# Optimization experiments

Measured on AMD Instinct MI355X. Metric: run time of the kernel, lower is better.

## Reference

```python
import jax, jax.numpy as jnp
import numpy as np

D = 8        # q_ndim (= dof_ndim)
HID = 200    # hidden_size
N = 16384    # batch of states
EPS = 0.1    # qdot regularizer coefficient in L()


def _lagrangian(z, Ws, bs):
    # z: (2D,) = [q, qdot]; angular_dims=() so CosSin is an identity pass-through
    v = z[D:]
    h = z
    for W, b in zip(Ws[:-1], bs[:-1]):
        h = jax.nn.softplus(h @ W + b)   # FCsoftplus blocks
    L = (h @ Ws[-1] + bs[-1])[0]          # final Linear -> scalar (Reshape(-1))
    return L + EPS * jnp.dot(v, v)


def setup_inputs():
    key = jax.random.key(0)
    ks = jax.random.split(key, 5)
    z = jax.random.normal(ks[0], (N, 2 * D), dtype=jnp.float32)
    t = jnp.zeros((), dtype=jnp.float32)

    def lin(k, fi, fo, scale):
        return (jax.random.normal(k, (fi, fo), dtype=jnp.float32)
                * jnp.float32(scale / np.sqrt(fi)))

    W0 = lin(ks[1], 2 * D, HID, 1.0)
    W1 = lin(ks[2], HID, HID, 1.0)
    W2 = lin(ks[3], HID, HID, 1.0)
    W3 = lin(ks[4], HID, 1, 0.01)  # small head keeps mass matrix M well conditioned
    b0 = jnp.zeros((HID,), jnp.float32)  # zero_bias init per FCsoftplus/Linear
    b1 = jnp.zeros((HID,), jnp.float32)
    b2 = jnp.zeros((HID,), jnp.float32)
    b3 = jnp.zeros((1,), jnp.float32)
    return dict(t=t, z=z, W0=W0, b0=b0, W1=W1, b1=b1, W2=W2, b2=b2, W3=W3, b3=b3)


def reference(t, z, W0, b0, W1, b1, W2, b2, W3, b3):
    # Euler-Lagrange dynamics (LagrangianDynamics):
    #   M a = dL/dq - (d2L/dq dv) v,  M = d2L/dv2;  dz/dt = [v, a]
    Ws = (W0, W1, W2, W3)
    bs = (b0, b1, b2, b3)
    Lfn = lambda zz: _lagrangian(zz, Ws, bs)

    def dyn_single(zi):
        g = jax.grad(Lfn)(zi)              # (2D,)  = [dL/dq, dL/dv]
        H = jax.jacfwd(jax.grad(Lfn))(zi)  # (2D,2D) Hessian of L wrt z
        v = zi[D:]
        M = H[D:, D:]                      # d(dL/dv)/dv  -> mass matrix
        C = H[D:, :D]                      # d(dL/dv)/dq
        F = g[:D] - C @ v
        a = jnp.linalg.solve(M, F)
        return jnp.concatenate([v, a])     # (2D,)

    return jax.vmap(dyn_single)(z)         # (N, 2D)
```

## Files before the change

kernel.cpp:

```cpp
#include <hip/hip_runtime.h>
#include <math.h>

#define DD 8
#define ZD 16
#define HID 200
#define EPSL 0.1f
#define BS 16
#define NTHREADS 512
#define NKC 7
#define NMT 13
#define XSTR 216
#define CSTR 212
#define HSTR 20
#define NTAN 8

#define KSC 1024.0f
#define SSC 64.0f
#define INV_K (1.0f/1024.0f)
#define INV_KS (1.0f/65536.0f)

typedef _Float16 half8 __attribute__((ext_vector_type(8)));
typedef _Float16 half4v __attribute__((ext_vector_type(4)));
typedef float float4v __attribute__((ext_vector_type(4)));

#define S4 (NKC*NMT*64*8)
#define OFF_W1T 0
#define OFF_W2T (S4)
#define OFF_W1  (2*S4)
#define OFF_W2  (3*S4)
#define OFF_W0T (4*S4)
#define OFF_W0  (4*S4 + NMT*64*8)
#define WS_HALFS (4*S4 + NMT*64*8 + NKC*64*8)

__global__ void prep(const float* __restrict__ W0, const float* __restrict__ W1,
                     const float* __restrict__ W2, _Float16* __restrict__ ws)
{
    int idx = blockIdx.x * 256 + threadIdx.x;
    if (idx >= WS_HALFS) return;
    float v = 0.f;
    if (idx < 4*S4) {
        int arr = idx / S4, e = idx % S4;
        int kc = e / (NMT*64*8); int r = e % (NMT*64*8);
        int mt = r / (64*8); r %= 64*8;
        int lane = r / 8, j = r % 8;
        int m = mt*16 + (lane & 15);
        int k = kc*32 + (lane >> 4)*8 + j;
        if (m < HID && k < HID) {
            if      (arr == 0) v = W1[k*HID + m];
            else if (arr == 1) v = W2[k*HID + m];
            else if (arr == 2) v = W1[m*HID + k];
            else               v = W2[m*HID + k];
        }
    } else if (idx < OFF_W0) {
        int e = idx - OFF_W0T;
        int mt = e / (64*8); int r = e % (64*8);
        int lane = r / 8, j = r % 8;
        int m = mt*16 + (lane & 15);
        int k = (lane >> 4)*8 + j;
        if (m < HID && k < ZD) v = W0[k*HID + m];
    } else {
        int e = idx - OFF_W0;
        int kc = e / (64*8); int r = e % (64*8);
        int lane = r / 8, j = r % 8;
        int m = (lane & 15);
        int k = kc*32 + (lane >> 4)*8 + j;
        if (k < HID) v = W0[m*HID + k];
    }
    ws[idx] = (_Float16)v;
}

__device__ __forceinline__ float4v ldc4(const _Float16* p) {
    half4v h = *(const half4v*)p;
    float4v f; f.x = (float)h.x; f.y = (float)h.y; f.z = (float)h.z; f.w = (float)h.w;
    return f;
}
__device__ __forceinline__ void sth4(_Float16* p, float a, float b, float c, float d) {
    half4v h; h.x = (_Float16)a; h.y = (_Float16)b; h.z = (_Float16)c; h.w = (_Float16)d;
    *(half4v*)p = h;
}
__device__ __forceinline__ void sig_sp(float x, float& sp, float& sg) {
    float e = __expf(-fabsf(x));
    float r = 1.0f / (1.0f + e);
    sg = (x >= 0.f) ? r : (1.0f - r);
    sp = fmaxf(x, 0.f) + __logf(1.f + e);
}

template<int NTILES>
__device__ __forceinline__ void run_mv(const half8* __restrict__ Asw,
                                       const _Float16* Xsrc,
                                       int mt0, int mtc, int lane,
                                       float4v acc[2][NTILES])
{
    const int lm = lane & 15, q = lane >> 4;
#pragma unroll
    for (int m = 0; m < 2; ++m)
#pragma unroll
        for (int n = 0; n < NTILES; ++n)
            acc[m][n] = (float4v){0.f, 0.f, 0.f, 0.f};
    for (int kc = 0; kc < NKC; ++kc) {
        half8 a[2];
#pragma unroll
        for (int m = 0; m < 2; ++m)
            if (m < mtc) a[m] = Asw[(kc*NMT + mt0 + m)*64 + lane];
        half8 x[NTILES];
#pragma unroll
        for (int n = 0; n < NTILES; ++n)
            x[n] = *(const half8*)(Xsrc + (n*16 + lm)*XSTR + kc*32 + q*8);
#pragma unroll
        for (int m = 0; m < 2; ++m)
            if (m < mtc)
#pragma unroll
                for (int n = 0; n < NTILES; ++n)
                    acc[m][n] = __builtin_amdgcn_mfma_f32_16x16x32_f16(a[m], x[n], acc[m][n], 0, 0, 0);
    }
}

__global__ void __launch_bounds__(NTHREADS, 1)
lnn_main(const float* __restrict__ z,
         const float* __restrict__ W0, const float* __restrict__ b0,
         const float* __restrict__ b1, const float* __restrict__ b2,
         const float* __restrict__ W3,
         const _Float16* __restrict__ ws,
         float* __restrict__ out)
{
    __shared__ _Float16 Xt[128*XSTR];
    __shared__ _Float16 Xb[128*XSTR];
    __shared__ _Float16 Cf[5][16*CSTR];
    __shared__ _Float16 Xz[16*40];
    __shared__ float gsh[16*HSTR];
    __shared__ float Hr[128*HSTR];

    const int tid  = threadIdx.x;
    const int wave = tid >> 6;
    const int lane = tid & 63;
    const int lm   = lane & 15;
    const int q    = lane >> 4;
    const int s0   = blockIdx.x * BS;

    const int mt0 = (wave < 5) ? wave*2 : (10 + (wave - 5));
    const int mtc = (wave < 5) ? 2 : 1;

    const half8* W1Tsw = (const half8*)(ws + OFF_W1T);
    const half8* W2Tsw = (const half8*)(ws + OFF_W2T);
    const half8* W1sw  = (const half8*)(ws + OFF_W1);
    const half8* W2sw  = (const half8*)(ws + OFF_W2);
    const half8* W0Tsw = (const half8*)(ws + OFF_W0T);
    const half8* W0sw  = (const half8*)(ws + OFF_W0);

    {
        if (tid < 256) {
            int s = tid >> 4, k = tid & 15;
            Xz[s*40 + k]      = (_Float16)z[(s0 + s)*ZD + k];
            Xz[s*40 + 16 + k] = (_Float16)0.f;
        }
        for (int idx = tid; idx < 128*16; idx += NTHREADS) {
            int r = idx >> 4, c = 200 + (idx & 15);
            Xt[r*XSTR + c] = (_Float16)0.f;
            Xb[r*XSTR + c] = (_Float16)0.f;
        }
    }
    __syncthreads();

    float4v acc1[2][1];

    {
#pragma unroll
        for (int m = 0; m < 2; ++m) acc1[m][0] = (float4v){0.f,0.f,0.f,0.f};
        half8 xz = *(const half8*)(Xz + lm*40 + q*8);
#pragma unroll
        for (int m = 0; m < 2; ++m)
            if (m < mtc) {
                half8 a = W0Tsw[(mt0 + m)*64 + lane];
                acc1[m][0] = __builtin_amdgcn_mfma_f32_16x16x32_f16(a, xz, acc1[m][0], 0, 0, 0);
            }
#pragma unroll
        for (int m = 0; m < 2; ++m)
            if (m < mtc) {
                int mt = mt0 + m, ub = mt*16 + q*4;
                bool pad = (mt == 12 && q >= 2);
                float4v bb = *(const float4v*)(b0 + ub);
                float h[4], p[4];
#pragma unroll
                for (int r = 0; r < 4; ++r) {
                    float a = acc1[m][0][r] + bb[r];
                    float sp, sg; sig_sp(a, sp, sg);
                    h[r] = pad ? 0.f : sp;
                    p[r] = pad ? 0.f : sg;
                }
                sth4(&Xt[lm*XSTR + ub], h[0], h[1], h[2], h[3]);
                sth4(&Cf[0][lm*CSTR + ub], p[0], p[1], p[2], p[3]);
            }
    }
    __syncthreads();

    run_mv<1>(W1Tsw, Xt, mt0, mtc, lane, acc1);
    __syncthreads();
#pragma unroll
    for (int m = 0; m < 2; ++m)
        if (m < mtc) {
            int mt = mt0 + m, ub = mt*16 + q*4;
            bool pad = (mt == 12 && q >= 2);
            float4v bb = *(const float4v*)(b1 + ub);
            float h[4], p[4];
#pragma unroll
            for (int r = 0; r < 4; ++r) {
                float a = acc1[m][0][r] + bb[r];
                float sp, sg; sig_sp(a, sp, sg);
                h[r] = pad ? 0.f : sp;
                p[r] = pad ? 0.f : sg;
            }
            sth4(&Xt[lm*XSTR + ub], h[0], h[1], h[2], h[3]);
            sth4(&Cf[1][lm*CSTR + ub], p[0], p[1], p[2], p[3]);
        }
    __syncthreads();

    run_mv<1>(W2Tsw, Xt, mt0, mtc, lane, acc1);
    __syncthreads();
#pragma unroll
    for (int m = 0; m < 2; ++m)
        if (m < mtc) {
            int mt = mt0 + m, ub = mt*16 + q*4;
            bool pad = (mt == 12 && q >= 2);
            float4v bb = *(const float4v*)(b2 + ub);
            float4v w3 = *(const float4v*)(W3 + ub);
            float d2[4], c2[4];
#pragma unroll
            for (int r = 0; r < 4; ++r) {
                float a = acc1[m][0][r] + bb[r];
                float e = __expf(-fabsf(a));
                float rr = 1.f / (1.f + e);
                float sg = (a >= 0.f) ? rr : (1.f - rr);
                float wk = KSC * w3[r];
                d2[r] = pad ? 0.f : wk * sg;
                c2[r] = pad ? 0.f : wk * sg * (1.f - sg);
            }
            sth4(&Xt[lm*XSTR + ub], d2[0], d2[1], d2[2], d2[3]);
            sth4(&Cf[2][lm*CSTR + ub], c2[0], c2[1], c2[2], c2[3]);
        }
    __syncthreads();

    run_mv<1>(W2sw, Xt, mt0, mtc, lane, acc1);
    __syncthreads();
#pragma unroll
    for (int m = 0; m < 2; ++m)
        if (m < mtc) {
            int mt = mt0 + m, ub = mt*16 + q*4;
            bool pad = (mt == 12 && q >= 2);
            float4v p1 = ldc4(&Cf[1][lm*CSTR + ub]);
            float d1[4], c3[4];
#pragma unroll
            for (int r = 0; r < 4; ++r) {
                float u1 = acc1[m][0][r];
                d1[r] = pad ? 0.f : u1 * p1[r];
                c3[r] = pad ? 0.f : u1 * (1.f - p1[r]);
            }
            sth4(&Xt[lm*XSTR + ub], d1[0], d1[1], d1[2], d1[3]);
            sth4(&Cf[3][lm*CSTR + ub], c3[0], c3[1], c3[2], c3[3]);
        }
    __syncthreads();

    run_mv<1>(W1sw, Xt, mt0, mtc, lane, acc1);
    __syncthreads();
#pragma unroll
    for (int m = 0; m < 2; ++m)
        if (m < mtc) {
            int mt = mt0 + m, ub = mt*16 + q*4;
            bool pad = (mt == 12 && q >= 2);
            float4v p0 = ldc4(&Cf[0][lm*CSTR + ub]);
            float d0[4], c4[4];
#pragma unroll
            for (int r = 0; r < 4; ++r) {
                float u0 = acc1[m][0][r];
                d0[r] = pad ? 0.f : u0 * p0[r];
                c4[r] = pad ? 0.f : u0 * p0[r] * (1.f - p0[r]);
            }
            sth4(&Xt[lm*XSTR + ub], d0[0], d0[1], d0[2], d0[3]);
            sth4(&Cf[4][lm*CSTR + ub], c4[0], c4[1], c4[2], c4[3]);
        }
    __syncthreads();

    if (wave == 0) {
        float4v g = (float4v){0.f,0.f,0.f,0.f};
        for (int kc = 0; kc < NKC; ++kc) {
            half8 a = W0sw[kc*64 + lane];
            half8 x = *(const half8*)(Xt + lm*XSTR + kc*32 + q*8);
            g = __builtin_amdgcn_mfma_f32_16x16x32_f16(a, x, g, 0, 0, 0);
        }
        float4v gv; gv.x = g.x*INV_K; gv.y = g.y*INV_K; gv.z = g.z*INV_K; gv.w = g.w*INV_K;
        *(float4v*)(&gsh[lm*HSTR + q*4]) = gv;
    }
    __syncthreads();

    for (int idx = tid; idx < 128*50; idx += NTHREADS) {
        int row = idx / 50, c4 = idx % 50;
        int u = c4 * 4;
        int t = row >> 4, s = row & 15;
        float4v p0 = ldc4(&Cf[0][s*CSTR + u]);
        float4v t0 = *(const float4v*)(W0 + (DD + t)*HID + u);
        sth4(&Xt[row*XSTR + u], SSC*p0.x*t0.x, SSC*p0.y*t0.y, SSC*p0.z*t0.z, SSC*p0.w*t0.w);
    }
    __syncthreads();

    float4v acc8[2][NTAN];

    run_mv<NTAN>(W1Tsw, Xt, mt0, mtc, lane, acc8);
    __syncthreads();
#pragma unroll
    for (int m = 0; m < 2; ++m)
        if (m < mtc) {
            int mt = mt0 + m, ub = mt*16 + q*4;
            bool pad = (mt == 12 && q >= 2);
            float4v p1 = ldc4(&Cf[1][lm*CSTR + ub]);
#pragma unroll
            for (int n = 0; n < NTAN; ++n) {
                int row = n*16 + lm;
                float a0 = pad ? 0.f : acc8[m][n][0]*p1[0];
                float a1 = pad ? 0.f : acc8[m][n][1]*p1[1];
                float a2 = pad ? 0.f : acc8[m][n][2]*p1[2];
                float a3 = pad ? 0.f : acc8[m][n][3]*p1[3];
                sth4(&Xb[row*XSTR + ub], a0, a1, a2, a3);
            }
        }
    __syncthreads();

    run_mv<NTAN>(W2Tsw, Xb, mt0, mtc, lane, acc8);
    __syncthreads();
#pragma unroll
    for (int m = 0; m < 2; ++m)
        if (m < mtc) {
            int mt = mt0 + m, ub = mt*16 + q*4;
            bool pad = (mt == 12 && q >= 2);
            float4v c2 = ldc4(&Cf[2][lm*CSTR + ub]);
#pragma unroll
            for (int n = 0; n < NTAN; ++n) {
                int row = n*16 + lm;
                float a0 = pad ? 0.f : acc8[m][n][0]*c2[0];
                float a1 = pad ? 0.f : acc8[m][n][1]*c2[1];
                float a2 = pad ? 0.f : acc8[m][n][2]*c2[2];
                float a3 = pad ? 0.f : acc8[m][n][3]*c2[3];
                sth4(&Xt[row*XSTR + ub], a0, a1, a2, a3);
            }
        }
    __syncthreads();

    run_mv<NTAN>(W2sw, Xt, mt0, mtc, lane, acc8);
    __syncthreads();
#pragma unroll
    for (int m = 0; m < 2; ++m)
        if (m < mtc) {
            int mt = mt0 + m, ub = mt*16 + q*4;
            bool pad = (mt == 12 && q >= 2);
            float4v p1 = ldc4(&Cf[1][lm*CSTR + ub]);
            float4v c3 = ldc4(&Cf[3][lm*CSTR + ub]);
#pragma unroll
            for (int n = 0; n < NTAN; ++n) {
                int row = n*16 + lm;
                float4v th1 = ldc4(&Xb[row*XSTR + ub]);
                float a0 = pad ? 0.f : acc8[m][n][0]*p1[0] + c3[0]*th1[0];
                float a1 = pad ? 0.f : acc8[m][n][1]*p1[1] + c3[1]*th1[1];
                float a2 = pad ? 0.f : acc8[m][n][2]*p1[2] + c3[2]*th1[2];
                float a3 = pad ? 0.f : acc8[m][n][3]*p1[3] + c3[3]*th1[3];
                sth4(&Xt[row*XSTR + ub], a0, a1, a2, a3);
            }
        }
    __syncthreads();

    run_mv<NTAN>(W1sw, Xt, mt0, mtc, lane, acc8);
    __syncthreads();
#pragma unroll
    for (int m = 0; m < 2; ++m)
        if (m < mtc) {
            int mt = mt0 + m, ub = mt*16 + q*4;
            bool pad = (mt == 12 && q >= 2);
            float4v p0 = ldc4(&Cf[0][lm*CSTR + ub]);
            float4v c4 = ldc4(&Cf[4][lm*CSTR + ub]);
#pragma unroll
            for (int n = 0; n < NTAN; ++n) {
                int row = n*16 + lm;
                float4v t0 = *(const float4v*)(W0 + (DD + n)*HID + ub);
                float a0 = pad ? 0.f : acc8[m][n][0]*p0[0] + c4[0]*(SSC*t0[0]);
                float a1 = pad ? 0.f : acc8[m][n][1]*p0[1] + c4[1]*(SSC*t0[1]);
                float a2 = pad ? 0.f : acc8[m][n][2]*p0[2] + c4[2]*(SSC*t0[2]);
                float a3 = pad ? 0.f : acc8[m][n][3]*p0[3] + c4[3]*(SSC*t0[3]);
                sth4(&Xb[row*XSTR + ub], a0, a1, a2, a3);
            }
        }
    __syncthreads();

    {
        float4v hacc = (float4v){0.f,0.f,0.f,0.f};
        for (int kc = 0; kc < NKC; ++kc) {
            half8 a = W0sw[kc*64 + lane];
            half8 x = *(const half8*)(Xb + (wave*16 + lm)*XSTR + kc*32 + q*8);
            hacc = __builtin_amdgcn_mfma_f32_16x16x32_f16(a, x, hacc, 0, 0, 0);
        }
        int row = wave*16 + lm;
        float4v hv;
        hv.x = hacc.x*INV_KS; hv.y = hacc.y*INV_KS;
        hv.z = hacc.z*INV_KS; hv.w = hacc.w*INV_KS;
        *(float4v*)(&Hr[row*HSTR + q*4]) = hv;
    }
    __syncthreads();

    if (tid < BS) {
        const int s = tid;
        float M[DD][DD], F[DD], v[DD], a[DD];
#pragma unroll
        for (int c = 0; c < DD; ++c) v[c] = z[(s0 + s)*ZD + DD + c];
#pragma unroll
        for (int r = 0; r < DD; ++r) {
            float f = gsh[s*HSTR + r];
#pragma unroll
            for (int c = 0; c < DD; ++c) {
                M[r][c] = Hr[(r*16 + s)*HSTR + DD + c] + ((r == c) ? 2.f*EPSL : 0.f);
                f -= Hr[(r*16 + s)*HSTR + c] * v[c];
            }
            F[r] = f;
        }
#pragma unroll
        for (int col = 0; col < DD; ++col) {
            const float inv = 1.f / M[col][col];
#pragma unroll
            for (int r = col + 1; r < DD; ++r) {
                const float fac = M[r][col] * inv;
#pragma unroll
                for (int c = col + 1; c < DD; ++c) M[r][c] -= fac * M[col][c];
                F[r] -= fac * F[col];
            }
        }
#pragma unroll
        for (int r = DD - 1; r >= 0; --r) {
            float ssum = F[r];
#pragma unroll
            for (int c = r + 1; c < DD; ++c) ssum -= M[r][c] * a[c];
            a[r] = ssum / M[r][r];
        }
        float* op = out + (size_t)(s0 + s)*ZD;
#pragma unroll
        for (int c = 0; c < DD; ++c) { op[c] = v[c]; op[DD + c] = a[c]; }
    }
}

extern "C" void kernel_launch(void* const* d_in, const int* in_sizes, int n_in,
                              void* d_out, int out_size, void* d_ws, size_t ws_size,
                              hipStream_t stream)
{
    const float* z  = (const float*)d_in[1];
    const float* W0 = (const float*)d_in[2];
    const float* b0 = (const float*)d_in[3];
    const float* W1 = (const float*)d_in[4];
    const float* b1 = (const float*)d_in[5];
    const float* W2 = (const float*)d_in[6];
    const float* b2 = (const float*)d_in[7];
    const float* W3 = (const float*)d_in[8];
    float* out = (float*)d_out;
    _Float16* ws = (_Float16*)d_ws;

    const int n = in_sizes[1] / (2*DD);

    prep<<<dim3((WS_HALFS + 255)/256), dim3(256), 0, stream>>>(W0, W1, W2, ws);
    lnn_main<<<dim3(n / BS), dim3(NTHREADS), 0, stream>>>(
        z, W0, b0, b1, b2, W3, ws, out);
}
```

Baseline: 187.1 us.

## Double threads per block, split tangent tiles across wave pairs, use packed fp16 epilogues

Raises the block to 1024 threads (16 waves) and splits the eight tangent tiles of the Hessian-vector passes into two halves, so each wave pair handles 4 tiles instead of 8. The scalar forward/backward passes now give one M-tile to each of 13 waves. Biases, the W3 head and the scaled W0 tangent rows are staged in LDS as fp16, and the epilogues use packed fp16 arithmetic with pkrtz conversion instead of fp32 math. The intent is more parallelism per block and fewer VALU and global-load costs, at the price of fp16 rounding in the epilogues and more barrier participants.

```diff
diff --git a/kernel.cpp b/kernel.cpp
--- a/kernel.cpp
+++ b/kernel.cpp
@@ -6,13 +6,15 @@
 #define HID 200
 #define EPSL 0.1f
 #define BS 16
-#define NTHREADS 512
+#define NTHREADS 1024
 #define NKC 7
 #define NMT 13
 #define XSTR 216
 #define CSTR 212
 #define HSTR 20
+#define WSTR 208
 #define NTAN 8
+#define NT4 4
 
 #define KSC 1024.0f
 #define SSC 64.0f
@@ -21,6 +23,8 @@
 
 typedef _Float16 half8 __attribute__((ext_vector_type(8)));
 typedef _Float16 half4v __attribute__((ext_vector_type(4)));
+typedef _Float16 half2v __attribute__((ext_vector_type(2)));
+typedef __fp16 fp16x2 __attribute__((ext_vector_type(2)));
 typedef float float4v __attribute__((ext_vector_type(4)));
 
 #define S4 (NKC*NMT*64*8)
@@ -69,14 +73,10 @@
     ws[idx] = (_Float16)v;
 }
 
-__device__ __forceinline__ float4v ldc4(const _Float16* p) {
-    half4v h = *(const half4v*)p;
-    float4v f; f.x = (float)h.x; f.y = (float)h.y; f.z = (float)h.z; f.w = (float)h.w;
-    return f;
-}
-__device__ __forceinline__ void sth4(_Float16* p, float a, float b, float c, float d) {
-    half4v h; h.x = (_Float16)a; h.y = (_Float16)b; h.z = (_Float16)c; h.w = (_Float16)d;
-    *(half4v*)p = h;
+__device__ __forceinline__ half4v pk4(float4v a) {
+    half2v lo = __builtin_bit_cast(half2v, __builtin_amdgcn_cvt_pkrtz(a.x, a.y));
+    half2v hi = __builtin_bit_cast(half2v, __builtin_amdgcn_cvt_pkrtz(a.z, a.w));
+    return __builtin_shufflevector(lo, hi, 0, 1, 2, 3);
 }
 __device__ __forceinline__ void sig_sp(float x, float& sp, float& sg) {
     float e = __expf(-fabsf(x));
@@ -87,7 +87,7 @@
 
 template<int NTILES>
 __device__ __forceinline__ void run_mv(const half8* __restrict__ Asw,
-                                       const _Float16* Xsrc,
+                                       const _Float16* __restrict__ Xsrc,
                                        int mt0, int mtc, int lane,
                                        float4v acc[2][NTILES])
 {
@@ -115,7 +115,7 @@
     }
 }
 
-__global__ void __launch_bounds__(NTHREADS, 1)
+__global__ void __launch_bounds__(NTHREADS, 4)
 lnn_main(const float* __restrict__ z,
          const float* __restrict__ W0, const float* __restrict__ b0,
          const float* __restrict__ b1, const float* __restrict__ b2,
@@ -123,12 +123,14 @@
          const _Float16* __restrict__ ws,
          float* __restrict__ out)
 {
-    __shared__ _Float16 Xt[128*XSTR];
-    __shared__ _Float16 Xb[128*XSTR];
-    __shared__ _Float16 Cf[5][16*CSTR];
-    __shared__ _Float16 Xz[16*40];
-    __shared__ float gsh[16*HSTR];
-    __shared__ float Hr[128*HSTR];
+    __shared__ alignas(16) _Float16 Xt[128*XSTR];
+    __shared__ alignas(16) _Float16 Xb[128*XSTR];
+    __shared__ alignas(16) _Float16 Cf[5][16*CSTR];
+    __shared__ alignas(16) _Float16 Xz[16*40];
+    __shared__ alignas(16) _Float16 bsh[4*WSTR];
+    __shared__ alignas(16) _Float16 w0t[NTAN*WSTR];
+    __shared__ alignas(16) float gsh[16*HSTR];
+    __shared__ alignas(16) float Hr[128*HSTR];
 
     const int tid  = threadIdx.x;
     const int wave = tid >> 6;
@@ -137,8 +139,10 @@
     const int q    = lane >> 4;
     const int s0   = blockIdx.x * BS;
 
-    const int mt0 = (wave < 5) ? wave*2 : (10 + (wave - 5));
-    const int mtc = (wave < 5) ? 2 : 1;
+    const int twm  = wave >> 1;
+    const int twn  = wave & 1;
+    const int mt0t = (twm < 5) ? twm*2 : (twm + 5);
+    const int mtct = (twm < 5) ? 2 : 1;
 
     const half8* W1Tsw = (const half8*)(ws + OFF_W1T);
     const half8* W2Tsw = (const half8*)(ws + OFF_W2T);
@@ -147,136 +151,110 @@
     const half8* W0Tsw = (const half8*)(ws + OFF_W0T);
     const half8* W0sw  = (const half8*)(ws + OFF_W0);
 
-    {
-        if (tid < 256) {
-            int s = tid >> 4, k = tid & 15;
-            Xz[s*40 + k]      = (_Float16)z[(s0 + s)*ZD + k];
-            Xz[s*40 + 16 + k] = (_Float16)0.f;
-        }
-        for (int idx = tid; idx < 128*16; idx += NTHREADS) {
-            int r = idx >> 4, c = 200 + (idx & 15);
-            Xt[r*XSTR + c] = (_Float16)0.f;
-            Xb[r*XSTR + c] = (_Float16)0.f;
-        }
+    if (tid < 256) {
+        int s = tid >> 4, k = tid & 15;
+        Xz[s*40 + k]      = (_Float16)z[(s0 + s)*ZD + k];
+        Xz[s*40 + 16 + k] = (_Float16)0.f;
+    }
+    for (int idx = tid; idx < 128*16; idx += NTHREADS) {
+        int r = idx >> 4, c = 200 + (idx & 15);
+        Xt[r*XSTR + c] = (_Float16)0.f;
+        Xb[r*XSTR + c] = (_Float16)0.f;
+    }
+    for (int idx = tid; idx < 4*WSTR; idx += NTHREADS) {
+        int l = idx / WSTR, u = idx % WSTR;
+        float v = 0.f;
+        if (u < HID) {
+            if      (l == 0) v = b0[u];
+            else if (l == 1) v = b1[u];
+            else if (l == 2) v = b2[u];
+            else             v = KSC * W3[u];
+        }
+        bsh[idx] = (_Float16)v;
+    }
+    for (int idx = tid; idx < NTAN*WSTR; idx += NTHREADS) {
+        int t = idx / WSTR, u = idx % WSTR;
+        w0t[idx] = (_Float16)((u < HID) ? SSC * W0[(DD + t)*HID + u] : 0.f);
     }
     __syncthreads();
 
     float4v acc1[2][1];
-
-    {
-#pragma unroll
-        for (int m = 0; m < 2; ++m) acc1[m][0] = (float4v){0.f,0.f,0.f,0.f};
+    const int ubf = wave*16 + q*4;
+
+    if (wave < NMT) {
+        acc1[0][0] = (float4v){0.f,0.f,0.f,0.f};
         half8 xz = *(const half8*)(Xz + lm*40 + q*8);
-#pragma unroll
-        for (int m = 0; m < 2; ++m)
-            if (m < mtc) {
-                half8 a = W0Tsw[(mt0 + m)*64 + lane];
-                acc1[m][0] = __builtin_amdgcn_mfma_f32_16x16x32_f16(a, xz, acc1[m][0], 0, 0, 0);
-            }
-#pragma unroll
-        for (int m = 0; m < 2; ++m)
-            if (m < mtc) {
-                int mt = mt0 + m, ub = mt*16 + q*4;
-                bool pad = (mt == 12 && q >= 2);
-                float4v bb = *(const float4v*)(b0 + ub);
-                float h[4], p[4];
-#pragma unroll
-                for (int r = 0; r < 4; ++r) {
-                    float a = acc1[m][0][r] + bb[r];
-                    float sp, sg; sig_sp(a, sp, sg);
-                    h[r] = pad ? 0.f : sp;
-                    p[r] = pad ? 0.f : sg;
-                }
-                sth4(&Xt[lm*XSTR + ub], h[0], h[1], h[2], h[3]);
-                sth4(&Cf[0][lm*CSTR + ub], p[0], p[1], p[2], p[3]);
-            }
-    }
-    __syncthreads();
-
-    run_mv<1>(W1Tsw, Xt, mt0, mtc, lane, acc1);
-    __syncthreads();
-#pragma unroll
-    for (int m = 0; m < 2; ++m)
-        if (m < mtc) {
-            int mt = mt0 + m, ub = mt*16 + q*4;
-            bool pad = (mt == 12 && q >= 2);
-            float4v bb = *(const float4v*)(b1 + ub);
-            float h[4], p[4];
-#pragma unroll
-            for (int r = 0; r < 4; ++r) {
-                float a = acc1[m][0][r] + bb[r];
-                float sp, sg; sig_sp(a, sp, sg);
-                h[r] = pad ? 0.f : sp;
-                p[r] = pad ? 0.f : sg;
-            }
-            sth4(&Xt[lm*XSTR + ub], h[0], h[1], h[2], h[3]);
-            sth4(&Cf[1][lm*CSTR + ub], p[0], p[1], p[2], p[3]);
-        }
-    __syncthreads();
-
-    run_mv<1>(W2Tsw, Xt, mt0, mtc, lane, acc1);
-    __syncthreads();
-#pragma unroll
-    for (int m = 0; m < 2; ++m)
-        if (m < mtc) {
-            int mt = mt0 + m, ub = mt*16 + q*4;
-            bool pad = (mt == 12 && q >= 2);
-            float4v bb = *(const float4v*)(b2 + ub);
-            float4v w3 = *(const float4v*)(W3 + ub);
-            float d2[4], c2[4];
-#pragma unroll
-            for (int r = 0; r < 4; ++r) {
-                float a = acc1[m][0][r] + bb[r];
-                float e = __expf(-fabsf(a));
-                float rr = 1.f / (1.f + e);
-                float sg = (a >= 0.f) ? rr : (1.f - rr);
-                float wk = KSC * w3[r];
-                d2[r] = pad ? 0.f : wk * sg;
-                c2[r] = pad ? 0.f : wk * sg * (1.f - sg);
-            }
-            sth4(&Xt[lm*XSTR + ub], d2[0], d2[1], d2[2], d2[3]);
-            sth4(&Cf[2][lm*CSTR + ub], c2[0], c2[1], c2[2], c2[3]);
-        }
-    __syncthreads();
-
-    run_mv<1>(W2sw, Xt, mt0, mtc, lane, acc1);
-    __syncthreads();
-#pragma unroll
-    for (int m = 0; m < 2; ++m)
-        if (m < mtc) {
-            int mt = mt0 + m, ub = mt*16 + q*4;
-            bool pad = (mt == 12 && q >= 2);
-            float4v p1 = ldc4(&Cf[1][lm*CSTR + ub]);
-            float d1[4], c3[4];
-#pragma unroll
-            for (int r = 0; r < 4; ++r) {
-                float u1 = acc1[m][0][r];
-                d1[r] = pad ? 0.f : u1 * p1[r];
-                c3[r] = pad ? 0.f : u1 * (1.f - p1[r]);
-            }
-            sth4(&Xt[lm*XSTR + ub], d1[0], d1[1], d1[2], d1[3]);
-            sth4(&Cf[3][lm*CSTR + ub], c3[0], c3[1], c3[2], c3[3]);
-        }
-    __syncthreads();
-
-    run_mv<1>(W1sw, Xt, mt0, mtc, lane, acc1);
-    __syncthreads();
-#pragma unroll
-    for (int m = 0; m < 2; ++m)
-        if (m < mtc) {
-            int mt = mt0 + m, ub = mt*16 + q*4;
-            bool pad = (mt == 12 && q >= 2);
-            float4v p0 = ldc4(&Cf[0][lm*CSTR + ub]);
-            float d0[4], c4[4];
-#pragma unroll
-            for (int r = 0; r < 4; ++r) {
-                float u0 = acc1[m][0][r];
-                d0[r] = pad ? 0.f : u0 * p0[r];
-                c4[r] = pad ? 0.f : u0 * p0[r] * (1.f - p0[r]);
-            }
-            sth4(&Xt[lm*XSTR + ub], d0[0], d0[1], d0[2], d0[3]);
-            sth4(&Cf[4][lm*CSTR + ub], c4[0], c4[1], c4[2], c4[3]);
-        }
+        half8 a = W0Tsw[wave*64 + lane];
+        acc1[0][0] = __builtin_amdgcn_mfma_f32_16x16x32_f16(a, xz, acc1[0][0], 0, 0, 0);
+        half4v bb = *(const half4v*)(&bsh[0*WSTR + ubf]);
+        float h[4], p[4];
+#pragma unroll
+        for (int r = 0; r < 4; ++r) {
+            float av = acc1[0][0][r] + (float)bb[r];
+            sig_sp(av, h[r], p[r]);
+        }
+        *(half4v*)(&Xt[lm*XSTR + ubf])     = pk4((float4v){h[0],h[1],h[2],h[3]});
+        *(half4v*)(&Cf[0][lm*CSTR + ubf])  = pk4((float4v){p[0],p[1],p[2],p[3]});
+    }
+    __syncthreads();
+
+    if (wave < NMT) run_mv<1>(W1Tsw, Xt, wave, 1, lane, acc1);
+    __syncthreads();
+    if (wave < NMT) {
+        half4v bb = *(const half4v*)(&bsh[1*WSTR + ubf]);
+        float h[4], p[4];
+#pragma unroll
+        for (int r = 0; r < 4; ++r) {
+            float av = acc1[0][0][r] + (float)bb[r];
+            sig_sp(av, h[r], p[r]);
+        }
+        *(half4v*)(&Xt[lm*XSTR + ubf])    = pk4((float4v){h[0],h[1],h[2],h[3]});
+        *(half4v*)(&Cf[1][lm*CSTR + ubf]) = pk4((float4v){p[0],p[1],p[2],p[3]});
+    }
+    __syncthreads();
+
+    if (wave < NMT) run_mv<1>(W2Tsw, Xt, wave, 1, lane, acc1);
+    __syncthreads();
+    if (wave < NMT) {
+        half4v bb = *(const half4v*)(&bsh[2*WSTR + ubf]);
+        half4v w3 = *(const half4v*)(&bsh[3*WSTR + ubf]);
+        float d2[4], c2[4];
+#pragma unroll
+        for (int r = 0; r < 4; ++r) {
+            float av = acc1[0][0][r] + (float)bb[r];
+            float e = __expf(-fabsf(av));
+            float rr = 1.f / (1.f + e);
+            float sg = (av >= 0.f) ? rr : (1.f - rr);
+            float wk = (float)w3[r];
+            d2[r] = wk * sg;
+            c2[r] = wk * sg * (1.f - sg);
+        }
+        *(half4v*)(&Xt[lm*XSTR + ubf])    = pk4((float4v){d2[0],d2[1],d2[2],d2[3]});
+        *(half4v*)(&Cf[2][lm*CSTR + ubf]) = pk4((float4v){c2[0],c2[1],c2[2],c2[3]});
+    }
+    __syncthreads();
+
+    if (wave < NMT) run_mv<1>(W2sw, Xt, wave, 1, lane, acc1);
+    __syncthreads();
+    if (wave < NMT) {
+        half4v p1 = *(const half4v*)(&Cf[1][lm*CSTR + ubf]);
+        half4v u1 = pk4(acc1[0][0]);
+        half4v one = {(_Float16)1.f,(_Float16)1.f,(_Float16)1.f,(_Float16)1.f};
+        *(half4v*)(&Xt[lm*XSTR + ubf])    = u1 * p1;
+        *(half4v*)(&Cf[3][lm*CSTR + ubf]) = u1 * (one - p1);
+    }
+    __syncthreads();
+
+    if (wave < NMT) run_mv<1>(W1sw, Xt, wave, 1, lane, acc1);
+    __syncthreads();
+    if (wave < NMT) {
+        half4v p0 = *(const half4v*)(&Cf[0][lm*CSTR + ubf]);
+        half4v u0 = pk4(acc1[0][0]);
+        half4v one = {(_Float16)1.f,(_Float16)1.f,(_Float16)1.f,(_Float16)1.f};
+        half4v d0 = u0 * p0;
+        *(half4v*)(&Xt[lm*XSTR + ubf])    = d0;
+        *(half4v*)(&Cf[4][lm*CSTR + ubf]) = d0 * (one - p0);
+    }
     __syncthreads();
 
     if (wave == 0) {
@@ -288,110 +266,88 @@
         }
         float4v gv; gv.x = g.x*INV_K; gv.y = g.y*INV_K; gv.z = g.z*INV_K; gv.w = g.w*INV_K;
         *(float4v*)(&gsh[lm*HSTR + q*4]) = gv;
-    }
-    __syncthreads();
-
-    for (int idx = tid; idx < 128*50; idx += NTHREADS) {
-        int row = idx / 50, c4 = idx % 50;
-        int u = c4 * 4;
-        int t = row >> 4, s = row & 15;
-        float4v p0 = ldc4(&Cf[0][s*CSTR + u]);
-        float4v t0 = *(const float4v*)(W0 + (DD + t)*HID + u);
-        sth4(&Xt[row*XSTR + u], SSC*p0.x*t0.x, SSC*p0.y*t0.y, SSC*p0.z*t0.z, SSC*p0.w*t0.w);
-    }
-    __syncthreads();
-
-    float4v acc8[2][NTAN];
-
-    run_mv<NTAN>(W1Tsw, Xt, mt0, mtc, lane, acc8);
+    } else {
+        for (int idx = tid - 64; idx < 128*50; idx += NTHREADS - 64) {
+            int row = idx / 50, u = (idx % 50)*4;
+            int s = row & 15, t = row >> 4;
+            half4v p0 = *(const half4v*)(&Cf[0][s*CSTR + u]);
+            half4v w0 = *(const half4v*)(&w0t[t*WSTR + u]);
+            *(half4v*)(&Xb[row*XSTR + u]) = p0 * w0;
+        }
+    }
+    __syncthreads();
+
+    float4v acc4[2][NT4];
+
+    run_mv<NT4>(W1Tsw, Xb + twn*64*XSTR, mt0t, mtct, lane, acc4);
     __syncthreads();
 #pragma unroll
     for (int m = 0; m < 2; ++m)
-        if (m < mtc) {
-            int mt = mt0 + m, ub = mt*16 + q*4;
-            bool pad = (mt == 12 && q >= 2);
-            float4v p1 = ldc4(&Cf[1][lm*CSTR + ub]);
-#pragma unroll
-            for (int n = 0; n < NTAN; ++n) {
-                int row = n*16 + lm;
-                float a0 = pad ? 0.f : acc8[m][n][0]*p1[0];
-                float a1 = pad ? 0.f : acc8[m][n][1]*p1[1];
-                float a2 = pad ? 0.f : acc8[m][n][2]*p1[2];
-                float a3 = pad ? 0.f : acc8[m][n][3]*p1[3];
-                sth4(&Xb[row*XSTR + ub], a0, a1, a2, a3);
-            }
-        }
-    __syncthreads();
-
-    run_mv<NTAN>(W2Tsw, Xb, mt0, mtc, lane, acc8);
+        if (m < mtct) {
+            const int ub = (mt0t + m)*16 + q*4;
+            half4v p1 = *(const half4v*)(&Cf[1][lm*CSTR + ub]);
+#pragma unroll
+            for (int n = 0; n < NT4; ++n) {
+                int row = (twn*NT4 + n)*16 + lm;
+                *(half4v*)(&Xt[row*XSTR + ub]) = pk4(acc4[m][n]) * p1;
+            }
+        }
+    __syncthreads();
+
+    run_mv<NT4>(W2Tsw, Xt + twn*64*XSTR, mt0t, mtct, lane, acc4);
     __syncthreads();
 #pragma unroll
     for (int m = 0; m < 2; ++m)
-        if (m < mtc) {
-            int mt = mt0 + m, ub = mt*16 + q*4;
-            bool pad = (mt == 12 && q >= 2);
-            float4v c2 = ldc4(&Cf[2][lm*CSTR + ub]);
-#pragma unroll
-            for (int n = 0; n < NTAN; ++n) {
-                int row = n*16 + lm;
-                float a0 = pad ? 0.f : acc8[m][n][0]*c2[0];
-                float a1 = pad ? 0.f : acc8[m][n][1]*c2[1];
-                float a2 = pad ? 0.f : acc8[m][n][2]*c2[2];
-                float a3 = pad ? 0.f : acc8[m][n][3]*c2[3];
-                sth4(&Xt[row*XSTR + ub], a0, a1, a2, a3);
-            }
-        }
-    __syncthreads();
-
-    run_mv<NTAN>(W2sw, Xt, mt0, mtc, lane, acc8);
+        if (m < mtct) {
+            const int ub = (mt0t + m)*16 + q*4;
+            half4v c2 = *(const half4v*)(&Cf[2][lm*CSTR + ub]);
+#pragma unroll
+            for (int n = 0; n < NT4; ++n) {
+                int row = (twn*NT4 + n)*16 + lm;
+                *(half4v*)(&Xb[row*XSTR + ub]) = pk4(acc4[m][n]) * c2;
+            }
+        }
+    __syncthreads();
+
+    run_mv<NT4>(W2sw, Xb + twn*64*XSTR, mt0t, mtct, lane, acc4);
     __syncthreads();
 #pragma unroll
     for (int m = 0; m < 2; ++m)
-        if (m < mtc) {
-            int mt = mt0 + m, ub = mt*16 + q*4;
-            bool pad = (mt == 12 && q >= 2);
-            float4v p1 = ldc4(&Cf[1][lm*CSTR + ub]);
-            float4v c3 = ldc4(&Cf[3][lm*CSTR + ub]);
-#pragma unroll
-            for (int n = 0; n < NTAN; ++n) {
-                int row = n*16 + lm;
-                float4v th1 = ldc4(&Xb[row*XSTR + ub]);
-                float a0 = pad ? 0.f : acc8[m][n][0]*p1[0] + c3[0]*th1[0];
-                float a1 = pad ? 0.f : acc8[m][n][1]*p1[1] + c3[1]*th1[1];
-                float a2 = pad ? 0.f : acc8[m][n][2]*p1[2] + c3[2]*th1[2];
-                float a3 = pad ? 0.f : acc8[m][n][3]*p1[3] + c3[3]*th1[3];
-                sth4(&Xt[row*XSTR + ub], a0, a1, a2, a3);
-            }
-        }
-    __syncthreads();
-
-    run_mv<NTAN>(W1sw, Xt, mt0, mtc, lane, acc8);
+        if (m < mtct) {
+            const int ub = (mt0t + m)*16 + q*4;
+            half4v p1 = *(const half4v*)(&Cf[1][lm*CSTR + ub]);
+            half4v c3 = *(const half4v*)(&Cf[3][lm*CSTR + ub]);
+#pragma unroll
+            for (int n = 0; n < NT4; ++n) {
+                int row = (twn*NT4 + n)*16 + lm;
+                half4v th1 = *(const half4v*)(&Xt[row*XSTR + ub]);
+                *(half4v*)(&Xb[row*XSTR + ub]) = pk4(acc4[m][n]) * p1 + c3 * th1;
+            }
+        }
+    __syncthreads();
+
+    run_mv<NT4>(W1sw, Xb + twn*64*XSTR, mt0t, mtct, lane, acc4);
     __syncthreads();
 #pragma unroll
     for (int m = 0; m < 2; ++m)
-        if (m < mtc) {
-            int mt = mt0 + m, ub = mt*16 + q*4;
-            bool pad = (mt == 12 && q >= 2);
-            float4v p0 = ldc4(&Cf[0][lm*CSTR + ub]);
-            float4v c4 = ldc4(&Cf[4][lm*CSTR + ub]);
-#pragma unroll
-            for (int n = 0; n < NTAN; ++n) {
-                int row = n*16 + lm;
-                float4v t0 = *(const float4v*)(W0 + (DD + n)*HID + ub);
-                float a0 = pad ? 0.f : acc8[m][n][0]*p0[0] + c4[0]*(SSC*t0[0]);
-                float a1 = pad ? 0.f : acc8[m][n][1]*p0[1] + c4[1]*(SSC*t0[1]);
-                float a2 = pad ? 0.f : acc8[m][n][2]*p0[2] + c4[2]*(SSC*t0[2]);
-                float a3 = pad ? 0.f : acc8[m][n][3]*p0[3] + c4[3]*(SSC*t0[3]);
-                sth4(&Xb[row*XSTR + ub], a0, a1, a2, a3);
-            }
-        }
-    __syncthreads();
-
-    {
+        if (m < mtct) {
+            const int ub = (mt0t + m)*16 + q*4;
+            half4v p0 = *(const half4v*)(&Cf[0][lm*CSTR + ub]);
+            half4v c4 = *(const half4v*)(&Cf[4][lm*CSTR + ub]);
+#pragma unroll
+            for (int n = 0; n < NT4; ++n) {
+                int row = (twn*NT4 + n)*16 + lm;
+                half4v w0 = *(const half4v*)(&w0t[(twn*NT4 + n)*WSTR + ub]);
+                *(half4v*)(&Xt[row*XSTR + ub]) = pk4(acc4[m][n]) * p0 + c4 * w0;
+            }
+        }
+    __syncthreads();
+
+    if (wave < 8) {
         float4v hacc = (float4v){0.f,0.f,0.f,0.f};
         for (int kc = 0; kc < NKC; ++kc) {
             half8 a = W0sw[kc*64 + lane];
-            half8 x = *(const half8*)(Xb + (wave*16 + lm)*XSTR + kc*32 + q*8);
+            half8 x = *(const half8*)(Xt + (wave*16 + lm)*XSTR + kc*32 + q*8);
             hacc = __builtin_amdgcn_mfma_f32_16x16x32_f16(a, x, hacc, 0, 0, 0);
         }
         int row = wave*16 + lm;
```

Result: faster. 159.9 us (-14.6%).
